# Kernel optimization log

Hardware: AMD Instinct MI355X
Metric: run time of the kernel (lower is better)

## Reference

```python
import jax, jax.numpy as jnp
import numpy as np

IN_U = 1024
OUT_U = 1024
BATCH = 4096
HID = 20            # ceil(log2(IN_U*OUT_U)), layer_encoding_dim=0 since num_layers=1
MLP_H = 10
FEAT = 3 + 3 * HID  # 63


def setup_inputs() -> dict:
    key = jax.random.key(0)
    ks = jax.random.split(key, 6)
    X = jax.random.normal(ks[0], (BATCH, IN_U), dtype=jnp.float32)
    weight = jax.random.normal(ks[1], (IN_U, OUT_U), dtype=jnp.float32) * 0.02
    # binary positional encodings per cell (encode_weight_hidden_states)
    k = jnp.arange(IN_U * OUT_U, dtype=jnp.int32).reshape(IN_U, OUT_U)
    shifts = jnp.arange(HID - 1, -1, -1, dtype=jnp.int32)
    hidden = ((k[..., None] >> shifts) & 1).astype(jnp.float32)  # [IN_U, OUT_U, HID]
    W1 = jax.random.normal(ks[2], (FEAT, MLP_H), dtype=jnp.float32) / np.float32(np.sqrt(FEAT))
    b1 = jnp.zeros((MLP_H,), jnp.float32)
    W2 = jax.random.normal(ks[3], (MLP_H, MLP_H), dtype=jnp.float32) / np.float32(np.sqrt(MLP_H))
    b2 = jnp.zeros((MLP_H,), jnp.float32)
    W3 = jax.random.normal(ks[4], (MLP_H, 1 + HID), dtype=jnp.float32) / np.float32(np.sqrt(MLP_H))
    b3 = jnp.zeros((1 + HID,), jnp.float32)
    return {"X": X, "weight": weight, "hidden": hidden,
            "W1": W1, "b1": b1, "W2": W2, "b2": b2, "W3": W3, "b3": b3}


def reference(X, weight, hidden, W1, b1, W2, b2, W3, b3):
    n, m = weight.shape
    # exclude-self column means ('forward') and row means ('backward')
    fwd_mean = (jnp.sum(weight, axis=0, keepdims=True) - weight) / (n - 1)   # [n,m]
    bwd_mean = (jnp.sum(weight, axis=1, keepdims=True) - weight) / (m - 1)   # [n,m]
    fwd_hs = (jnp.sum(hidden, axis=0, keepdims=True) - hidden) / (n - 1)     # [n,m,H]
    bwd_hs = (jnp.sum(hidden, axis=1, keepdims=True) - hidden) / (m - 1)     # [n,m,H]
    feat = jnp.concatenate(
        [weight[..., None], fwd_mean[..., None], bwd_mean[..., None],
         hidden, fwd_hs, bwd_hs], axis=-1)                                   # [n,m,3+3H]
    h = jax.nn.relu(jnp.einsum('nmf,fh->nmh', feat, W1) + b1)
    h = jax.nn.relu(jnp.einsum('nmh,hk->nmk', h, W2) + b2)
    updates = jnp.einsum('nmk,ko->nmo', h, W3) + b3                          # [n,m,1+H]
    new_weight = weight + updates[..., 0]
    # (hidden states also get updates[...,1:] in the torch module, but only the
    #  softmax output is returned)
    logits = jax.nn.relu(X @ new_weight)                                     # [B,m]
    return jax.nn.softmax(logits, axis=-1)
```

## Files before the change

### kernel.cpp

```cpp
#include <hip/hip_runtime.h>
#include <hip/hip_bf16.h>
#include <stdint.h>


#define RS_OFF      0
#define CSPART_OFF  4096
#define BT_OFF      266240
#define AH_OFF      2363392

typedef __attribute__((ext_vector_type(8))) _Float16 f16x8;
typedef __attribute__((ext_vector_type(4))) float f32x4;

__device__ __forceinline__ unsigned short f2h(float x) {
    _Float16 h = (_Float16)x;
    unsigned short u;
    __builtin_memcpy(&u, &h, 2);
    return u;
}
__device__ __forceinline__ void gld16(const void* g, void* l) {
    __builtin_amdgcn_global_load_lds(
        (const __attribute__((address_space(1))) unsigned*)g,
        (__attribute__((address_space(3))) unsigned*)l, 16, 0, 0);
}

__global__ __launch_bounds__(256) void k_pre(const float* __restrict__ w,
        float* __restrict__ rs, float* __restrict__ cs_part) {
    __shared__ float part[4][1024];
    int t = threadIdx.x;
    int lane = t & 63, wv = t >> 6;
    int r0 = blockIdx.x * 16 + wv * 4;
    float ccol[16];
    #pragma unroll
    for (int j = 0; j < 16; ++j) ccol[j] = 0.f;
    #pragma unroll
    for (int rr = 0; rr < 4; ++rr) {
        int row = r0 + rr;
        float rsum = 0.f;
        #pragma unroll
        for (int j = 0; j < 16; ++j) {
            float v = w[(size_t)row * 1024 + j * 64 + lane];
            ccol[j] += v;
            rsum += v;
        }
        #pragma unroll
        for (int o = 32; o; o >>= 1) rsum += __shfl_down(rsum, o);
        if (lane == 0) rs[row] = rsum;
    }
    #pragma unroll
    for (int j = 0; j < 16; ++j) part[wv][j * 64 + lane] = ccol[j];
    __syncthreads();
    #pragma unroll
    for (int j = 0; j < 4; ++j) {
        int c = t + j * 256;
        cs_part[(size_t)blockIdx.x * 1024 + c] =
            part[0][c] + part[1][c] + part[2][c] + part[3][c];
    }
}

__global__ __launch_bounds__(256) void k_nw(const float* __restrict__ w,
        const float* __restrict__ X,
        const float* __restrict__ rs, const float* __restrict__ cs_part,
        const float* __restrict__ W1, const float* __restrict__ b1,
        const float* __restrict__ W2, const float* __restrict__ b2,
        const float* __restrict__ W3, const float* __restrict__ b3,
        unsigned short* __restrict__ Bt, unsigned short* __restrict__ Ah) {
    __shared__ float sW1[630], sW2[100], sb1[10], sb2[10], sw3[10], sa[10];
    __shared__ float rs_loc[32], cs_loc[32];
    __shared__ float rn_loc[320], cm_loc[320];
    __shared__ float st[32][33];
    int t = threadIdx.x;
    if (blockIdx.x >= 1024) {
        int b2x = blockIdx.x - 1024;
        #pragma unroll
        for (int p = 0; p < 4; ++p) {
            size_t idx = (size_t)b2x * 4096 + p * 1024 + t * 4;
            float4 v = *(const float4*)&X[idx];
            ushort4 h;
            h.x = f2h(v.x); h.y = f2h(v.y); h.z = f2h(v.z); h.w = f2h(v.w);
            *(ushort4*)&Ah[idx] = h;
        }
        return;
    }
    int n0 = (blockIdx.x & 31) * 32;
    int m0 = (blockIdx.x >> 5) * 32;
    const float inv = 1.0f / 1023.0f;

    for (int i = t; i < 630; i += 256) sW1[i] = W1[i];
    if (t < 100) sW2[t] = W2[t];
    if (t >= 128 && t < 138) { sb1[t - 128] = b1[t - 128]; sb2[t - 128] = b2[t - 128]; }
    if (t >= 160 && t < 170) sw3[t - 160] = W3[(t - 160) * 21];
    if (t >= 192 && t < 224) rs_loc[t - 192] = rs[n0 + t - 192];
    if (t >= 224 && t < 256) {
        float s = 0.f;
        #pragma unroll
        for (int p = 0; p < 64; ++p) s += cs_part[(size_t)p * 1024 + m0 + (t - 224)];
        cs_loc[t - 224] = s;
    }
    float b30 = b3[0];
    __syncthreads();
    if (t < 10) sa[t] = sW1[t] - (sW1[10 + t] + sW1[20 + t]) * inv;
    for (int id = t; id < 640; id += 256) {
        int h = id % 10, i = (id / 10) & 31, side = id >= 320;
        if (!side) {
            int n = n0 + i;
            float v = rs_loc[i] * sW1[20 + h] * inv;
            #pragma unroll
            for (int j = 0; j < 10; j++) {
                float bit = (float)((n >> (9 - j)) & 1);
                v += bit * (sW1[(3 + j) * 10 + h] + sW1[(43 + j) * 10 + h]
                            - sW1[(23 + j) * 10 + h] * inv);
                v += (512.0f * inv) * sW1[(23 + j) * 10 + h];
            }
            rn_loc[i * 10 + h] = v;
        } else {
            int m = m0 + i;
            float v = cs_loc[i] * sW1[10 + h] * inv + sb1[h];
            #pragma unroll
            for (int j = 0; j < 10; j++) {
                float bit = (float)((m >> (9 - j)) & 1);
                v += bit * (sW1[(13 + j) * 10 + h] + sW1[(33 + j) * 10 + h]
                            - sW1[(53 + j) * 10 + h] * inv);
                v += (512.0f * inv) * sW1[(53 + j) * 10 + h];
            }
            cm_loc[i * 10 + h] = v;
        }
    }
    __syncthreads();
    int ml = t & 31;
    #pragma unroll
    for (int i = 0; i < 4; i++) {
        int nl = (t >> 5) + 8 * i;
        float wv = w[(size_t)(n0 + nl) * 1024 + m0 + ml];
        float h1[10];
        #pragma unroll
        for (int h = 0; h < 10; h++)
            h1[h] = fmaxf(wv * sa[h] + rn_loc[nl * 10 + h] + cm_loc[ml * 10 + h], 0.f);
        float u = b30;
        #pragma unroll
        for (int k = 0; k < 10; k++) {
            float h2 = sb2[k];
            #pragma unroll
            for (int h = 0; h < 10; h++) h2 += h1[h] * sW2[h * 10 + k];
            u += fmaxf(h2, 0.f) * sw3[k];
        }
        st[nl][ml] = wv + u;
    }
    __syncthreads();
    int mrow = t >> 3, kc = t & 7;
    unsigned short hi4[4];
    #pragma unroll
    for (int j = 0; j < 4; j++)
        hi4[j] = f2h(st[kc * 4 + j][mrow]);
    size_t base = (size_t)(m0 + mrow) * 1024 + n0 + kc * 4;
    *(ushort4*)&Bt[base] = make_ushort4(hi4[0], hi4[1], hi4[2], hi4[3]);
}

__global__ __launch_bounds__(256, 3) void k_gemm9(const unsigned short* __restrict__ Ah,
        const unsigned short* __restrict__ Bt, float* __restrict__ out) {
    __shared__ unsigned short sAh[128 * 64];
    __shared__ unsigned short sBh[64 * 64];
    int tid = threadIdx.x;
    int lane = tid & 63, w = tid >> 6;
    int b = blockIdx.x;
    int xcd = b & 7, s = b >> 3;
    int ty = (xcd << 2) | (s >> 4);
    int tx = s & 15;
    int n0 = tx * 64, m0 = ty * 128;
    int wm = (w >> 1) * 64, wn = (w & 1) * 32;
    int quad = lane >> 4, l16 = lane & 15;

    f32x4 acc[4][2];
    #pragma unroll
    for (int i = 0; i < 4; i++)
        #pragma unroll
        for (int j = 0; j < 2; j++) acc[i][j] = (f32x4)0.f;

    for (int it = 0; it < 16; ++it) {
        int kb = it * 64;
        __syncthreads();
        #pragma unroll
        for (int s2 = 0; s2 < 4; ++s2) {
            int P = s2 * 256 + tid;
            int row = P >> 3;
            int seg = (P & 7) ^ (row & 7);
            int ldsOff = (s2 * 256 + w * 64) * 8;
            size_t ga = (size_t)(m0 + row) * 1024 + kb + seg * 8;
            gld16(&Ah[ga], &sAh[ldsOff]);
        }
        #pragma unroll
        for (int s2 = 0; s2 < 2; ++s2) {
            int P = s2 * 256 + tid;
            int row = P >> 3;
            int seg = (P & 7) ^ (row & 7);
            int ldsOff = (s2 * 256 + w * 64) * 8;
            size_t gb = (size_t)(n0 + row) * 1024 + kb + seg * 8;
            gld16(&Bt[gb], &sBh[ldsOff]);
        }
        __syncthreads();
        #pragma unroll
        for (int ks = 0; ks < 2; ++ks) {
            int segk = ks * 4 + quad;
            f16x8 ah[4], bh[2];
            #pragma unroll
            for (int i = 0; i < 4; ++i) {
                int ra = wm + i * 16 + l16;
                int ca = (ra * 8 + (segk ^ (ra & 7))) * 8;
                ah[i] = *(const f16x8*)&sAh[ca];
            }
            #pragma unroll
            for (int j = 0; j < 2; ++j) {
                int rb = wn + j * 16 + l16;
                int cb = (rb * 8 + (segk ^ (rb & 7))) * 8;
                bh[j] = *(const f16x8*)&sBh[cb];
            }
            #pragma unroll
            for (int i = 0; i < 4; ++i)
                #pragma unroll
                for (int j = 0; j < 2; ++j)
                    acc[i][j] = __builtin_amdgcn_mfma_f32_16x16x32_f16(ah[i], bh[j], acc[i][j], 0, 0, 0);
        }
    }
    #pragma unroll
    for (int i = 0; i < 4; ++i) {
        int mr = m0 + wm + i * 16 + quad * 4;
        #pragma unroll
        for (int j = 0; j < 2; ++j) {
            int nc = n0 + wn + j * 16 + l16;
            #pragma unroll
            for (int r = 0; r < 4; ++r)
                out[(size_t)(mr + r) * 1024 + nc] = fmaxf(acc[i][j][r], 0.f);
        }
    }
}

__global__ __launch_bounds__(256) void k_softmax2(float* __restrict__ C) {
    int row = blockIdx.x, t = threadIdx.x, lane = t & 63, wv = t >> 6;
    __shared__ float red[8];
    float4 v = *(float4*)&C[(size_t)row * 1024 + t * 4];
    float lm = fmaxf(fmaxf(v.x, v.y), fmaxf(v.z, v.w));
    #pragma unroll
    for (int o = 32; o; o >>= 1) lm = fmaxf(lm, __shfl_down(lm, o));
    if (lane == 0) red[wv] = lm;
    __syncthreads();
    float mx = fmaxf(fmaxf(red[0], red[1]), fmaxf(red[2], red[3]));
    float4 e;
    e.x = __expf(v.x - mx); e.y = __expf(v.y - mx);
    e.z = __expf(v.z - mx); e.w = __expf(v.w - mx);
    float ls = e.x + e.y + e.z + e.w;
    #pragma unroll
    for (int o = 32; o; o >>= 1) ls += __shfl_down(ls, o);
    if (lane == 0) red[4 + wv] = ls;
    __syncthreads();
    float inv = 1.0f / (red[4] + red[5] + red[6] + red[7]);
    e.x *= inv; e.y *= inv; e.z *= inv; e.w *= inv;
    *(float4*)&C[(size_t)row * 1024 + t * 4] = e;
}

extern "C" void kernel_launch(void* const* d_in, const int* in_sizes, int n_in,
                              void* d_out, int out_size, void* d_ws, size_t ws_size,
                              hipStream_t stream) {
    const float* X  = (const float*)d_in[0];
    const float* W  = (const float*)d_in[1];
    const float* W1 = (const float*)d_in[3];
    const float* b1 = (const float*)d_in[4];
    const float* W2 = (const float*)d_in[5];
    const float* b2 = (const float*)d_in[6];
    const float* W3 = (const float*)d_in[7];
    const float* b3 = (const float*)d_in[8];

    char* wsb = (char*)d_ws;
    float* rs            = (float*)(wsb + RS_OFF);
    float* cs_part       = (float*)(wsb + CSPART_OFF);
    unsigned short* Bt   = (unsigned short*)(wsb + BT_OFF);
    unsigned short* Ah   = (unsigned short*)(wsb + AH_OFF);
    float* out = (float*)d_out;

    k_pre<<<64, 256, 0, stream>>>(W, rs, cs_part);
    k_nw<<<2048, 256, 0, stream>>>(W, X, rs, cs_part, W1, b1, W2, b2, W3, b3, Bt, Ah);
    k_gemm9<<<512, 256, 0, stream>>>(Ah, Bt, out);
    k_softmax2<<<4096, 256, 0, stream>>>(out);
}
```

Baseline: 177.1 us.

## Double-buffer LDS tiles in GEMM to overlap global loads with MFMA

The GEMM kernel now keeps two LDS buffers for the A and B tiles. While it computes on the current tile, it prefetches the next K-tile with global_load_lds, which removes one barrier per iteration. The aim is to hide global-to-LDS latency behind MFMA work. LDS use doubles and launch bounds drop from 3 to 2 blocks per CU, which may reduce occupancy-based latency hiding.

```diff
diff --git a/kernel.cpp b/kernel.cpp
--- a/kernel.cpp
+++ b/kernel.cpp
@@ -155,10 +155,10 @@
     *(ushort4*)&Bt[base] = make_ushort4(hi4[0], hi4[1], hi4[2], hi4[3]);
 }
 
-__global__ __launch_bounds__(256, 3) void k_gemm9(const unsigned short* __restrict__ Ah,
+__global__ __launch_bounds__(256, 2) void k_gemm10(const unsigned short* __restrict__ Ah,
         const unsigned short* __restrict__ Bt, float* __restrict__ out) {
-    __shared__ unsigned short sAh[128 * 64];
-    __shared__ unsigned short sBh[64 * 64];
+    __shared__ unsigned short sAh[2][128 * 64];
+    __shared__ unsigned short sBh[2][64 * 64];
     int tid = threadIdx.x;
     int lane = tid & 63, w = tid >> 6;
     int b = blockIdx.x;
@@ -175,28 +175,35 @@
         #pragma unroll
         for (int j = 0; j < 2; j++) acc[i][j] = (f32x4)0.f;
 
+#define STAGE_TILE(kb, buf)                                                  \
+    do {                                                                     \
+        _Pragma("unroll")                                                    \
+        for (int s2 = 0; s2 < 4; ++s2) {                                     \
+            int P = s2 * 256 + tid;                                          \
+            int row = P >> 3;                                                \
+            int seg = (P & 7) ^ (row & 7);                                   \
+            int ldsOff = (s2 * 256 + w * 64) * 8;      \
+            size_t ga = (size_t)(m0 + row) * 1024 + (kb) + seg * 8;          \
+            gld16(&Ah[ga], &sAh[buf][ldsOff]);                               \
+        }                                                                    \
+        _Pragma("unroll")                                                    \
+        for (int s2 = 0; s2 < 2; ++s2) {                                     \
+            int P = s2 * 256 + tid;                                          \
+            int row = P >> 3;                                                \
+            int seg = (P & 7) ^ (row & 7);                                   \
+            int ldsOff = (s2 * 256 + w * 64) * 8;                            \
+            size_t gb = (size_t)(n0 + row) * 1024 + (kb) + seg * 8;          \
+            gld16(&Bt[gb], &sBh[buf][ldsOff]);                               \
+        }                                                                    \
+    } while (0)
+
+    STAGE_TILE(0, 0);
+    __syncthreads();
+
+    #pragma unroll 2
     for (int it = 0; it < 16; ++it) {
-        int kb = it * 64;
-        __syncthreads();
-        #pragma unroll
-        for (int s2 = 0; s2 < 4; ++s2) {
-            int P = s2 * 256 + tid;
-            int row = P >> 3;
-            int seg = (P & 7) ^ (row & 7);
-            int ldsOff = (s2 * 256 + w * 64) * 8;
-            size_t ga = (size_t)(m0 + row) * 1024 + kb + seg * 8;
-            gld16(&Ah[ga], &sAh[ldsOff]);
-        }
-        #pragma unroll
-        for (int s2 = 0; s2 < 2; ++s2) {
-            int P = s2 * 256 + tid;
-            int row = P >> 3;
-            int seg = (P & 7) ^ (row & 7);
-            int ldsOff = (s2 * 256 + w * 64) * 8;
-            size_t gb = (size_t)(n0 + row) * 1024 + kb + seg * 8;
-            gld16(&Bt[gb], &sBh[ldsOff]);
-        }
-        __syncthreads();
+        int cur = it & 1;
+        if (it < 15) STAGE_TILE((it + 1) * 64, cur ^ 1);
         #pragma unroll
         for (int ks = 0; ks < 2; ++ks) {
             int segk = ks * 4 + quad;
@@ -205,13 +212,13 @@
             for (int i = 0; i < 4; ++i) {
                 int ra = wm + i * 16 + l16;
                 int ca = (ra * 8 + (segk ^ (ra & 7))) * 8;
-                ah[i] = *(const f16x8*)&sAh[ca];
+                ah[i] = *(const f16x8*)&sAh[cur][ca];
             }
             #pragma unroll
             for (int j = 0; j < 2; ++j) {
                 int rb = wn + j * 16 + l16;
                 int cb = (rb * 8 + (segk ^ (rb & 7))) * 8;
-                bh[j] = *(const f16x8*)&sBh[cb];
+                bh[j] = *(const f16x8*)&sBh[cur][cb];
             }
             #pragma unroll
             for (int i = 0; i < 4; ++i)
@@ -219,7 +226,10 @@
                 for (int j = 0; j < 2; ++j)
                     acc[i][j] = __builtin_amdgcn_mfma_f32_16x16x32_f16(ah[i], bh[j], acc[i][j], 0, 0, 0);
         }
-    }
+        if (it < 15) __syncthreads();
+    }
+#undef STAGE_TILE
+
     #pragma unroll
     for (int i = 0; i < 4; ++i) {
         int mr = m0 + wm + i * 16 + quad * 4;
@@ -277,6 +287,6 @@
 
     k_pre<<<64, 256, 0, stream>>>(W, rs, cs_part);
     k_nw<<<2048, 256, 0, stream>>>(W, X, rs, cs_part, W1, b1, W2, b2, W3, b3, Bt, Ah);
-    k_gemm9<<<512, 256, 0, stream>>>(Ah, Bt, out);
+    k_gemm10<<<512, 256, 0, stream>>>(Ah, Bt, out);
     k_softmax2<<<4096, 256, 0, stream>>>(out);
 }
```

After: 178.5 us. No clear change (+0.8%).
